# Kernel tuning notes

Measured on AMD Instinct MI355X. Metric: run time of the kernel, lower is better.

## Reference

```python
import jax, jax.numpy as jnp
import numpy as np

N, T, V = 256, 70, 64
B, H, C = 6, 1024, 4  # n_blocks, n_internal_units, n_class
SPECTRAL_RADIUS = 0.99
INPUT_SCALING = 0.2


def setup_inputs() -> dict:
    key = jax.random.key(0)
    k1, k2, k3, k4 = jax.random.split(key, 4)
    X = jax.random.normal(k1, (N, T, V), dtype=jnp.float32)
    # spectral-radius-normalized reservoir weights (circular law: rho(G/sqrt(H)) ~ 1)
    W_res = jax.random.normal(k2, (B, H, H), dtype=jnp.float32) * (SPECTRAL_RADIUS / jnp.sqrt(H).astype(jnp.float32))
    # +/-1 Bernoulli input weights scaled by input_scaling
    W_in = jnp.sign(jax.random.normal(k3, (B, H, V), dtype=jnp.float32)) * INPUT_SCALING
    W_lin = jax.random.normal(k4, (T, C, B * H), dtype=jnp.float32) * 0.02
    b_lin = jnp.zeros((T, C), dtype=jnp.float32)
    return {"X": X, "W_res": W_res, "W_in": W_in, "W_lin": W_lin, "b_lin": b_lin}


def reference(X, W_res, W_in, W_lin, b_lin):
    # Echo state recurrence: s_t = tanh(W_res @ s_{t-1} + W_in @ x_t), per block
    # (leak=None, noise_level=0.0, n_drop=0 as in module defaults)
    n, t_len, v = X.shape
    b, h, _ = W_res.shape

    def step(s, x_t):  # s: [B,N,H], x_t: [N,V]
        pre = jnp.einsum('bij,bnj->bni', W_res, s) + jnp.einsum('bhv,nv->bnh', W_in, x_t)
        s_new = jnp.tanh(pre)
        return s_new, s_new

    s0 = jnp.zeros((b, n, h), dtype=X.dtype)
    _, states = jax.lax.scan(step, s0, jnp.swapaxes(X, 0, 1))  # [T,B,N,H]

    # per-timestep features: concat blocks -> [T,N,B*H]
    feats = jnp.transpose(states, (0, 2, 1, 3)).reshape(t_len, n, b * h)
    # per-timestep linear heads
    logits = jnp.einsum('tnf,tcf->tnc', feats, W_lin) + b_lin[:, None, :]  # [T,N,C]
    preds = jnp.argmax(logits, axis=-1)  # [T,N], matches forward()'s class_dict
    return logits, preds
```

## Files before the change

### kernel.cpp

```cpp
#include <hip/hip_runtime.h>
#include <stdint.h>


typedef _Float16 f16;
typedef _Float16 f16x8 __attribute__((ext_vector_type(8)));
typedef float floatx4 __attribute__((ext_vector_type(4)));

#define N_TOT 256
#define T_TOT 70
#define V_TOT 64
#define B_TOT 6
#define H_TOT 1024
#define C_TOT 4
#define F_TOT (B_TOT * H_TOT)
#define G_TOT 192
#define LO_SCALE 4096.0f
#define LO_INV   (1.0f / 4096.0f)

union H8 { f16 h[8]; uint4 v; };

#define GLOAD16(g, l)                                                        \
    __builtin_amdgcn_global_load_lds(                                        \
        (const __attribute__((address_space(1))) void*)(g),                  \
        (__attribute__((address_space(3))) void*)(l), 16, 0, 0)

__global__ __launch_bounds__(256)
void split_f32(const float* __restrict__ src, f16* __restrict__ hi,
               f16* __restrict__ lo, int n)
{
    const int i = (blockIdx.x * 256 + threadIdx.x) * 8;
    if (i + 8 > n) return;
    const float4 a = *(const float4*)&src[i];
    const float4 b = *(const float4*)&src[i + 4];
    const float x[8] = {a.x, a.y, a.z, a.w, b.x, b.y, b.z, b.w};
    H8 H, L;
#pragma unroll
    for (int j = 0; j < 8; ++j) {
        const f16 h = (f16)x[j];
        H.h[j] = h;
        L.h[j] = (f16)((x[j] - (float)h) * LO_SCALE);
    }
    *(uint4*)&hi[i] = H.v;
    *(uint4*)&lo[i] = L.v;
}

__global__ __launch_bounds__(256)
void head_reduce(const float* __restrict__ part,
                 const float* __restrict__ b_lin,
                 float* __restrict__ logits,
                 float* __restrict__ preds)
{
    const int t = blockIdx.x;
    const int n = threadIdx.x;

    float a0 = b_lin[t * C_TOT + 0];
    float a1 = b_lin[t * C_TOT + 1];
    float a2 = b_lin[t * C_TOT + 2];
    float a3 = b_lin[t * C_TOT + 3];

    const float* p = part + (((size_t)t * G_TOT) * N_TOT + n) * C_TOT;
    for (int g = 0; g < G_TOT; ++g) {
        const float4 v = *(const float4*)&p[(size_t)g * N_TOT * C_TOT];
        a0 += v.x; a1 += v.y; a2 += v.z; a3 += v.w;
    }

    float4 o = {a0, a1, a2, a3};
    *(float4*)&logits[((size_t)t * N_TOT + n) * C_TOT] = o;

    int arg = 0;
    float best = a0;
    if (a1 > best) { best = a1; arg = 1; }
    if (a2 > best) { best = a2; arg = 2; }
    if (a3 > best) { best = a3; arg = 3; }
    preds[(size_t)t * N_TOT + n] = (float)arg;
}

__global__ __launch_bounds__(256)
void esn_step_fused(const f16* __restrict__ Xhi,   const f16* __restrict__ Xlo,
                    const f16* __restrict__ Whi,   const f16* __restrict__ Wlo,
                    const f16* __restrict__ Wihi,  const f16* __restrict__ Wilo,
                    const f16* __restrict__ shi_p, const f16* __restrict__ slo_p,
                    f16* __restrict__ shi_n,       f16* __restrict__ slo_n,
                    const float* __restrict__ W_lin, float* __restrict__ part,
                    int t, int first)
{
    __shared__ f16 As_hi[2][64 * 64];
    __shared__ f16 As_lo[2][64 * 64];
    __shared__ f16 Bs_hi[2][32 * 64];
    __shared__ f16 Bs_lo[2][32 * 64];

    const int p   = blockIdx.x;
    const int l   = (p & 7) * 96 + (p >> 3);
    const int mt  = l & 3;
    const int bi  = l >> 2;
    const int b   = bi >> 5;
    const int it  = bi & 31;

    const int tid  = threadIdx.x;
    const int w    = tid >> 6;
    const int lane = tid & 63;
    const int l16  = lane & 15;
    const int oct  = lane >> 4;
    const int r8   = lane >> 3;
    const int sw   = ((lane & 7) ^ r8) << 3;

    const int dA0 = (w * 16) * 64;
    const int dA1 = (w * 16 + 8) * 64;
    const int dB  = (w * 8) * 64;

    const int arow0 = mt * 64 + w * 16 + r8;
    const int arow1 = arow0 + 8;
    const int brow  = it * 32 + w * 8 + r8;

    const f16* Ah0 = shi_p + (size_t)(b * N_TOT + arow0) * H_TOT + sw;
    const f16* Ah1 = shi_p + (size_t)(b * N_TOT + arow1) * H_TOT + sw;
    const f16* Al0 = slo_p + (size_t)(b * N_TOT + arow0) * H_TOT + sw;
    const f16* Al1 = slo_p + (size_t)(b * N_TOT + arow1) * H_TOT + sw;
    const f16* Bh0 = Whi   + (size_t)(b * H_TOT + brow) * H_TOT + sw;
    const f16* Bl0 = Wlo   + (size_t)(b * H_TOT + brow) * H_TOT + sw;
    const f16* Xh0 = Xhi + ((size_t)arow0 * T_TOT + t) * V_TOT + sw;
    const f16* Xh1 = Xhi + ((size_t)arow1 * T_TOT + t) * V_TOT + sw;
    const f16* Xl0 = Xlo + ((size_t)arow0 * T_TOT + t) * V_TOT + sw;
    const f16* Xl1 = Xlo + ((size_t)arow1 * T_TOT + t) * V_TOT + sw;
    const f16* Wih = Wihi + (size_t)(b * H_TOT + brow) * V_TOT + sw;
    const f16* Wil = Wilo + (size_t)(b * H_TOT + brow) * V_TOT + sw;

    auto STAGE = [&](int k) {
        const int bb = k & 1;
        if (k < 16) {
            const size_t off = (size_t)k * 64;
            GLOAD16(Ah0 + off, &As_hi[bb][dA0]);
            GLOAD16(Ah1 + off, &As_hi[bb][dA1]);
            GLOAD16(Al0 + off, &As_lo[bb][dA0]);
            GLOAD16(Al1 + off, &As_lo[bb][dA1]);
            GLOAD16(Bh0 + off, &Bs_hi[bb][dB]);
            GLOAD16(Bl0 + off, &Bs_lo[bb][dB]);
        } else {
            GLOAD16(Xh0, &As_hi[bb][dA0]);
            GLOAD16(Xh1, &As_hi[bb][dA1]);
            GLOAD16(Xl0, &As_lo[bb][dA0]);
            GLOAD16(Xl1, &As_lo[bb][dA1]);
            GLOAD16(Wih, &Bs_hi[bb][dB]);
            GLOAD16(Wil, &Bs_lo[bb][dB]);
        }
    };

    floatx4 acc[2], accl[2];
#pragma unroll
    for (int j = 0; j < 2; ++j) { acc[j] = (floatx4)(0.0f); accl[j] = (floatx4)(0.0f); }

    const int xsw = (l16 & 7) << 3;
    const int aoff[2] = {
        (w * 16 + l16) * 64 + ((0 + oct * 8) ^ xsw),
        (w * 16 + l16) * 64 + ((32 + oct * 8) ^ xsw)
    };
    int boff[2][2];
#pragma unroll
    for (int nf = 0; nf < 2; ++nf) {
        boff[nf][0] = (nf * 16 + l16) * 64 + ((0 + oct * 8) ^ xsw);
        boff[nf][1] = (nf * 16 + l16) * 64 + ((32 + oct * 8) ^ xsw);
    }

    const int kc0 = first ? 16 : 0;
    STAGE(kc0);
    __syncthreads();

    for (int kc = kc0; kc <= 16; ++kc) {
        const int bb = kc & 1;
        if (kc < 16) STAGE(kc + 1);

#pragma unroll
        for (int half = 0; half < 2; ++half) {
            const f16x8 ah = *(const f16x8*)&As_hi[bb][aoff[half]];
            const f16x8 al = *(const f16x8*)&As_lo[bb][aoff[half]];
#pragma unroll
            for (int nf = 0; nf < 2; ++nf) {
                const f16x8 bh = *(const f16x8*)&Bs_hi[bb][boff[nf][half]];
                const f16x8 bl = *(const f16x8*)&Bs_lo[bb][boff[nf][half]];
                acc[nf]  = __builtin_amdgcn_mfma_f32_16x16x32_f16(ah, bh, acc[nf], 0, 0, 0);
                accl[nf] = __builtin_amdgcn_mfma_f32_16x16x32_f16(ah, bl, accl[nf], 0, 0, 0);
                accl[nf] = __builtin_amdgcn_mfma_f32_16x16x32_f16(al, bh, accl[nf], 0, 0, 0);
            }
        }
        if (kc < 16) __syncthreads();
    }

    const int nbase = mt * 64;
    const int ibase = it * 32;

    const float* wl = W_lin + (size_t)t * C_TOT * F_TOT + b * H_TOT + ibase;
    float wv[4][2];
#pragma unroll
    for (int c = 0; c < 4; ++c)
#pragma unroll
        for (int nf = 0; nf < 2; ++nf)
            wv[c][nf] = wl[(size_t)c * F_TOT + nf * 16 + l16];

    float sval[2][4];
#pragma unroll
    for (int nf = 0; nf < 2; ++nf)
#pragma unroll
        for (int r = 0; r < 4; ++r) {
            const int m  = w * 16 + oct * 4 + r;
            const int ii = nf * 16 + l16;
            const float s = tanhf(acc[nf][r] + accl[nf][r] * LO_INV);
            sval[nf][r] = s;
            const f16 h = (f16)s;
            const size_t oidx = (size_t)(b * N_TOT + nbase + m) * H_TOT + ibase + ii;
            shi_n[oidx] = h;
            slo_n[oidx] = (f16)((s - (float)h) * LO_SCALE);
        }

    const int g = b * 32 + it;
#pragma unroll
    for (int r = 0; r < 4; ++r) {
        float v[4];
#pragma unroll
        for (int c = 0; c < 4; ++c) {
            float x = sval[0][r] * wv[c][0] + sval[1][r] * wv[c][1];
            x += __shfl_xor(x, 1);
            x += __shfl_xor(x, 2);
            x += __shfl_xor(x, 4);
            x += __shfl_xor(x, 8);
            v[c] = x;
        }
        if (l16 == 0) {
            const int n = nbase + w * 16 + oct * 4 + r;
            float4 o = {v[0], v[1], v[2], v[3]};
            *(float4*)&part[(((size_t)t * G_TOT + g) * N_TOT + n) * C_TOT] = o;
        }
    }
}

extern "C" void kernel_launch(void* const* d_in, const int* in_sizes, int n_in,
                              void* d_out, int out_size, void* d_ws, size_t ws_size,
                              hipStream_t stream) {
    const float* X     = (const float*)d_in[0];
    const float* W_res = (const float*)d_in[1];
    const float* W_in  = (const float*)d_in[2];
    const float* W_lin = (const float*)d_in[3];
    const float* b_lin = (const float*)d_in[4];

    float* out    = (float*)d_out;
    float* logits = out;
    float* preds  = out + (size_t)T_TOT * N_TOT * C_TOT;

    const size_t nWres = (size_t)B_TOT * H_TOT * H_TOT;
    const size_t nWin  = (size_t)B_TOT * H_TOT * V_TOT;
    const size_t nX    = (size_t)N_TOT * T_TOT * V_TOT;
    const size_t nS    = (size_t)B_TOT * N_TOT * H_TOT;

    f16* p    = (f16*)d_ws;
    f16* Whi  = p;  p += nWres;
    f16* Wlo  = p;  p += nWres;
    f16* Wihi = p;  p += nWin;
    f16* Wilo = p;  p += nWin;
    f16* Xhi  = p;  p += nX;
    f16* Xlo  = p;  p += nX;
    f16* sAh  = p;  p += nS;
    f16* sAl  = p;  p += nS;
    f16* sBh  = p;  p += nS;
    f16* sBl  = p;  p += nS;
    float* part = (float*)p;

    split_f32<<<(int)(nWres / 2048), 256, 0, stream>>>(W_res, Whi, Wlo, (int)nWres);
    split_f32<<<(int)(nWin  / 2048), 256, 0, stream>>>(W_in, Wihi, Wilo, (int)nWin);
    split_f32<<<(int)(nX    / 2048), 256, 0, stream>>>(X, Xhi, Xlo, (int)nX);

    for (int t = 0; t < T_TOT; ++t) {
        const f16 *ph, *pl;
        f16 *nh, *nl;
        if (t & 1) { ph = sBh; pl = sBl; nh = sAh; nl = sAl; }
        else       { ph = sAh; pl = sAl; nh = sBh; nl = sBl; }
        esn_step_fused<<<B_TOT * 4 * 32, 256, 0, stream>>>(
            Xhi, Xlo, Whi, Wlo, Wihi, Wilo, ph, pl, nh, nl,
            W_lin, part, t, t == 0 ? 1 : 0);
    }
    head_reduce<<<T_TOT, 256, 0, stream>>>(part, b_lin, logits, preds);
}
```

Baseline: 1.511 ms.

## Enlarge per-block tile to 64x64 with 2-wave blocks and 2x4 MFMA fragments

```diff
diff --git a/kernel.cpp b/kernel.cpp
--- a/kernel.cpp
+++ b/kernel.cpp
@@ -75,7 +75,8 @@
     preds[(size_t)t * N_TOT + n] = (float)arg;
 }
 
-__global__ __launch_bounds__(256)
+__global__ __launch_bounds__(128)
+__attribute__((amdgpu_waves_per_eu(1, 2)))
 void esn_step_fused(const f16* __restrict__ Xhi,   const f16* __restrict__ Xlo,
                     const f16* __restrict__ Whi,   const f16* __restrict__ Wlo,
                     const f16* __restrict__ Wihi,  const f16* __restrict__ Wilo,
@@ -86,15 +87,15 @@
 {
     __shared__ f16 As_hi[2][64 * 64];
     __shared__ f16 As_lo[2][64 * 64];
-    __shared__ f16 Bs_hi[2][32 * 64];
-    __shared__ f16 Bs_lo[2][32 * 64];
+    __shared__ f16 Bs_hi[2][64 * 64];
+    __shared__ f16 Bs_lo[2][64 * 64];
 
     const int p   = blockIdx.x;
-    const int l   = (p & 7) * 96 + (p >> 3);
+    const int l   = (p & 7) * 48 + (p >> 3);
     const int mt  = l & 3;
     const int bi  = l >> 2;
-    const int b   = bi >> 5;
-    const int it  = bi & 31;
+    const int b   = bi >> 4;
+    const int it  = bi & 15;
 
     const int tid  = threadIdx.x;
     const int w    = tid >> 6;
@@ -104,62 +105,53 @@
     const int r8   = lane >> 3;
     const int sw   = ((lane & 7) ^ r8) << 3;
 
-    const int dA0 = (w * 16) * 64;
-    const int dA1 = (w * 16 + 8) * 64;
-    const int dB  = (w * 8) * 64;
-
-    const int arow0 = mt * 64 + w * 16 + r8;
-    const int arow1 = arow0 + 8;
-    const int brow  = it * 32 + w * 8 + r8;
-
-    const f16* Ah0 = shi_p + (size_t)(b * N_TOT + arow0) * H_TOT + sw;
-    const f16* Ah1 = shi_p + (size_t)(b * N_TOT + arow1) * H_TOT + sw;
-    const f16* Al0 = slo_p + (size_t)(b * N_TOT + arow0) * H_TOT + sw;
-    const f16* Al1 = slo_p + (size_t)(b * N_TOT + arow1) * H_TOT + sw;
-    const f16* Bh0 = Whi   + (size_t)(b * H_TOT + brow) * H_TOT + sw;
-    const f16* Bl0 = Wlo   + (size_t)(b * H_TOT + brow) * H_TOT + sw;
-    const f16* Xh0 = Xhi + ((size_t)arow0 * T_TOT + t) * V_TOT + sw;
-    const f16* Xh1 = Xhi + ((size_t)arow1 * T_TOT + t) * V_TOT + sw;
-    const f16* Xl0 = Xlo + ((size_t)arow0 * T_TOT + t) * V_TOT + sw;
-    const f16* Xl1 = Xlo + ((size_t)arow1 * T_TOT + t) * V_TOT + sw;
-    const f16* Wih = Wihi + (size_t)(b * H_TOT + brow) * V_TOT + sw;
-    const f16* Wil = Wilo + (size_t)(b * H_TOT + brow) * V_TOT + sw;
+    const f16* Ah  = shi_p + (size_t)(b * N_TOT + mt * 64 + w * 32 + r8) * H_TOT + sw;
+    const f16* Al  = slo_p + (size_t)(b * N_TOT + mt * 64 + w * 32 + r8) * H_TOT + sw;
+    const f16* Bh  = Whi   + (size_t)(b * H_TOT + it * 64 + w * 32 + r8) * H_TOT + sw;
+    const f16* Bl  = Wlo   + (size_t)(b * H_TOT + it * 64 + w * 32 + r8) * H_TOT + sw;
+    const f16* Xh  = Xhi + ((size_t)(mt * 64 + w * 32 + r8) * T_TOT + t) * V_TOT + sw;
+    const f16* Xl  = Xlo + ((size_t)(mt * 64 + w * 32 + r8) * T_TOT + t) * V_TOT + sw;
+    const f16* Wih = Wihi + (size_t)(b * H_TOT + it * 64 + w * 32 + r8) * V_TOT + sw;
+    const f16* Wil = Wilo + (size_t)(b * H_TOT + it * 64 + w * 32 + r8) * V_TOT + sw;
 
     auto STAGE = [&](int k) {
         const int bb = k & 1;
         if (k < 16) {
             const size_t off = (size_t)k * 64;
-            GLOAD16(Ah0 + off, &As_hi[bb][dA0]);
-            GLOAD16(Ah1 + off, &As_hi[bb][dA1]);
-            GLOAD16(Al0 + off, &As_lo[bb][dA0]);
-            GLOAD16(Al1 + off, &As_lo[bb][dA1]);
-            GLOAD16(Bh0 + off, &Bs_hi[bb][dB]);
-            GLOAD16(Bl0 + off, &Bs_lo[bb][dB]);
+#pragma unroll
+            for (int s = 0; s < 4; ++s) {
+                const int d = (w * 32 + s * 8) * 64;
+                GLOAD16(Ah + (size_t)s * 8 * H_TOT + off, &As_hi[bb][d]);
+                GLOAD16(Al + (size_t)s * 8 * H_TOT + off, &As_lo[bb][d]);
+                GLOAD16(Bh + (size_t)s * 8 * H_TOT + off, &Bs_hi[bb][d]);
+                GLOAD16(Bl + (size_t)s * 8 * H_TOT + off, &Bs_lo[bb][d]);
+            }
         } else {
-            GLOAD16(Xh0, &As_hi[bb][dA0]);
-            GLOAD16(Xh1, &As_hi[bb][dA1]);
-            GLOAD16(Xl0, &As_lo[bb][dA0]);
-            GLOAD16(Xl1, &As_lo[bb][dA1]);
-            GLOAD16(Wih, &Bs_hi[bb][dB]);
-            GLOAD16(Wil, &Bs_lo[bb][dB]);
+#pragma unroll
+            for (int s = 0; s < 4; ++s) {
+                const int d = (w * 32 + s * 8) * 64;
+                GLOAD16(Xh  + (size_t)s * 8 * T_TOT * V_TOT, &As_hi[bb][d]);
+                GLOAD16(Xl  + (size_t)s * 8 * T_TOT * V_TOT, &As_lo[bb][d]);
+                GLOAD16(Wih + (size_t)s * 8 * V_TOT,         &Bs_hi[bb][d]);
+                GLOAD16(Wil + (size_t)s * 8 * V_TOT,         &Bs_lo[bb][d]);
+            }
         }
     };
 
-    floatx4 acc[2], accl[2];
-#pragma unroll
-    for (int j = 0; j < 2; ++j) { acc[j] = (floatx4)(0.0f); accl[j] = (floatx4)(0.0f); }
+    floatx4 acc[2][4], accl[2][4];
+#pragma unroll
+    for (int m = 0; m < 2; ++m)
+#pragma unroll
+        for (int nf = 0; nf < 4; ++nf) {
+            acc[m][nf] = (floatx4)(0.0f);
+            accl[m][nf] = (floatx4)(0.0f);
+        }
 
     const int xsw = (l16 & 7) << 3;
-    const int aoff[2] = {
-        (w * 16 + l16) * 64 + ((0 + oct * 8) ^ xsw),
-        (w * 16 + l16) * 64 + ((32 + oct * 8) ^ xsw)
-    };
-    int boff[2][2];
-#pragma unroll
-    for (int nf = 0; nf < 2; ++nf) {
-        boff[nf][0] = (nf * 16 + l16) * 64 + ((0 + oct * 8) ^ xsw);
-        boff[nf][1] = (nf * 16 + l16) * 64 + ((32 + oct * 8) ^ xsw);
-    }
+    const int arow_lds[2] = { (w * 32 + l16) * 64, (w * 32 + 16 + l16) * 64 };
+    const int brow_lds[4] = { l16 * 64, (16 + l16) * 64,
+                              (32 + l16) * 64, (48 + l16) * 64 };
+    const int colk[2] = { (0 + oct * 8) ^ xsw, (32 + oct * 8) ^ xsw };
 
     const int kc0 = first ? 16 : 0;
     STAGE(kc0);
@@ -171,64 +163,79 @@
 
 #pragma unroll
         for (int half = 0; half < 2; ++half) {
-            const f16x8 ah = *(const f16x8*)&As_hi[bb][aoff[half]];
-            const f16x8 al = *(const f16x8*)&As_lo[bb][aoff[half]];
-#pragma unroll
-            for (int nf = 0; nf < 2; ++nf) {
-                const f16x8 bh = *(const f16x8*)&Bs_hi[bb][boff[nf][half]];
-                const f16x8 bl = *(const f16x8*)&Bs_lo[bb][boff[nf][half]];
-                acc[nf]  = __builtin_amdgcn_mfma_f32_16x16x32_f16(ah, bh, acc[nf], 0, 0, 0);
-                accl[nf] = __builtin_amdgcn_mfma_f32_16x16x32_f16(ah, bl, accl[nf], 0, 0, 0);
-                accl[nf] = __builtin_amdgcn_mfma_f32_16x16x32_f16(al, bh, accl[nf], 0, 0, 0);
+            f16x8 ah[2], al[2];
+#pragma unroll
+            for (int m = 0; m < 2; ++m) {
+                ah[m] = *(const f16x8*)&As_hi[bb][arow_lds[m] + colk[half]];
+                al[m] = *(const f16x8*)&As_lo[bb][arow_lds[m] + colk[half]];
+            }
+#pragma unroll
+            for (int nf = 0; nf < 4; ++nf) {
+                const f16x8 bh = *(const f16x8*)&Bs_hi[bb][brow_lds[nf] + colk[half]];
+                const f16x8 bl = *(const f16x8*)&Bs_lo[bb][brow_lds[nf] + colk[half]];
+#pragma unroll
+                for (int m = 0; m < 2; ++m) {
+                    acc[m][nf]  = __builtin_amdgcn_mfma_f32_16x16x32_f16(ah[m], bh, acc[m][nf], 0, 0, 0);
+                    accl[m][nf] = __builtin_amdgcn_mfma_f32_16x16x32_f16(ah[m], bl, accl[m][nf], 0, 0, 0);
+                    accl[m][nf] = __builtin_amdgcn_mfma_f32_16x16x32_f16(al[m], bh, accl[m][nf], 0, 0, 0);
+                }
             }
         }
         if (kc < 16) __syncthreads();
     }
 
     const int nbase = mt * 64;
-    const int ibase = it * 32;
+    const int ibase = it * 64;
 
     const float* wl = W_lin + (size_t)t * C_TOT * F_TOT + b * H_TOT + ibase;
-    float wv[4][2];
+    float wv[4][4];
 #pragma unroll
     for (int c = 0; c < 4; ++c)
 #pragma unroll
-        for (int nf = 0; nf < 2; ++nf)
+        for (int nf = 0; nf < 4; ++nf)
             wv[c][nf] = wl[(size_t)c * F_TOT + nf * 16 + l16];
 
-    float sval[2][4];
-#pragma unroll
-    for (int nf = 0; nf < 2; ++nf)
-#pragma unroll
-        for (int r = 0; r < 4; ++r) {
-            const int m  = w * 16 + oct * 4 + r;
-            const int ii = nf * 16 + l16;
-            const float s = tanhf(acc[nf][r] + accl[nf][r] * LO_INV);
-            sval[nf][r] = s;
-            const f16 h = (f16)s;
-            const size_t oidx = (size_t)(b * N_TOT + nbase + m) * H_TOT + ibase + ii;
-            shi_n[oidx] = h;
-            slo_n[oidx] = (f16)((s - (float)h) * LO_SCALE);
-        }
-
-    const int g = b * 32 + it;
-#pragma unroll
-    for (int r = 0; r < 4; ++r) {
-        float v[4];
-#pragma unroll
-        for (int c = 0; c < 4; ++c) {
-            float x = sval[0][r] * wv[c][0] + sval[1][r] * wv[c][1];
-            x += __shfl_xor(x, 1);
-            x += __shfl_xor(x, 2);
-            x += __shfl_xor(x, 4);
-            x += __shfl_xor(x, 8);
-            v[c] = x;
-        }
-        if (l16 == 0) {
-            const int n = nbase + w * 16 + oct * 4 + r;
-            float4 o = {v[0], v[1], v[2], v[3]};
-            *(float4*)&part[(((size_t)t * G_TOT + g) * N_TOT + n) * C_TOT] = o;
-        }
+    float sval[2][4][4];
+#pragma unroll
+    for (int m = 0; m < 2; ++m)
+#pragma unroll
+        for (int nf = 0; nf < 4; ++nf)
+#pragma unroll
+            for (int r = 0; r < 4; ++r) {
+                const int mrow = w * 32 + m * 16 + oct * 4 + r;
+                const int ii   = nf * 16 + l16;
+                const float s = tanhf(acc[m][nf][r] + accl[m][nf][r] * LO_INV);
+                sval[m][nf][r] = s;
+                const f16 h = (f16)s;
+                const size_t oidx = (size_t)(b * N_TOT + nbase + mrow) * H_TOT + ibase + ii;
+                shi_n[oidx] = h;
+                slo_n[oidx] = (f16)((s - (float)h) * LO_SCALE);
+            }
+
+#pragma unroll
+    for (int cg = 0; cg < 2; ++cg) {
+        const int g = b * 32 + it * 2 + cg;
+#pragma unroll
+        for (int m = 0; m < 2; ++m)
+#pragma unroll
+            for (int r = 0; r < 4; ++r) {
+                float v[4];
+#pragma unroll
+                for (int c = 0; c < 4; ++c) {
+                    float x = sval[m][2 * cg][r] * wv[c][2 * cg]
+                            + sval[m][2 * cg + 1][r] * wv[c][2 * cg + 1];
+                    x += __shfl_xor(x, 1);
+                    x += __shfl_xor(x, 2);
+                    x += __shfl_xor(x, 4);
+                    x += __shfl_xor(x, 8);
+                    v[c] = x;
+                }
+                if (l16 == 0) {
+                    const int n = nbase + w * 32 + m * 16 + oct * 4 + r;
+                    float4 o = {v[0], v[1], v[2], v[3]};
+                    *(float4*)&part[(((size_t)t * G_TOT + g) * N_TOT + n) * C_TOT] = o;
+                }
+            }
     }
 }
 
@@ -272,7 +279,7 @@
         f16 *nh, *nl;
         if (t & 1) { ph = sBh; pl = sBl; nh = sAh; nl = sAl; }
         else       { ph = sAh; pl = sAl; nh = sBh; nl = sBl; }
-        esn_step_fused<<<B_TOT * 4 * 32, 256, 0, stream>>>(
+        esn_step_fused<<<B_TOT * 16 * 4, 128, 0, stream>>>(
             Xhi, Xlo, Whi, Wlo, Wihi, Wilo, ph, pl, nh, nl,
             W_lin, part, t, t == 0 ? 1 : 0);
     }
```

New measurement: 2.305 ms. 52.6% more time.

## Interleave W hi/lo chunks and deepen the LDS pipeline to four stages

Applied to the files above, without the earlier changes.

```diff
diff --git a/kernel.cpp b/kernel.cpp
--- a/kernel.cpp
+++ b/kernel.cpp
@@ -24,6 +24,14 @@
         (const __attribute__((address_space(1))) void*)(g),                  \
         (__attribute__((address_space(3))) void*)(l), 16, 0, 0)
 
+#define LDSBAR(N)                                                            \
+    do {                                                                     \
+        __builtin_amdgcn_sched_barrier(0);                                   \
+        asm volatile("s_waitcnt vmcnt(" #N ") lgkmcnt(0)" ::: "memory");     \
+        __builtin_amdgcn_s_barrier();                                        \
+        __builtin_amdgcn_sched_barrier(0);                                   \
+    } while (0)
+
 __global__ __launch_bounds__(256)
 void split_f32(const float* __restrict__ src, f16* __restrict__ hi,
                f16* __restrict__ lo, int n)
@@ -45,6 +53,29 @@
 }
 
 __global__ __launch_bounds__(256)
+void csplit32(const float* __restrict__ src, f16* __restrict__ dst,
+              int n, int K)
+{
+    const int i = (blockIdx.x * 256 + threadIdx.x) * 8;
+    if (i + 8 > n) return;
+    const float4 a = *(const float4*)&src[i];
+    const float4 b = *(const float4*)&src[i + 4];
+    const float x[8] = {a.x, a.y, a.z, a.w, b.x, b.y, b.z, b.w};
+    H8 H, L;
+#pragma unroll
+    for (int j = 0; j < 8; ++j) {
+        const f16 h = (f16)x[j];
+        H.h[j] = h;
+        L.h[j] = (f16)((x[j] - (float)h) * LO_SCALE);
+    }
+    const int row = i / K;
+    const int k   = i - row * K;
+    const size_t o = ((size_t)row * (K >> 5) + (k >> 5)) * 64 + (k & 31);
+    *(uint4*)&dst[o]      = H.v;
+    *(uint4*)&dst[o + 32] = L.v;
+}
+
+__global__ __launch_bounds__(256)
 void head_reduce(const float* __restrict__ part,
                  const float* __restrict__ b_lin,
                  float* __restrict__ logits,
@@ -77,17 +108,15 @@
 
 __global__ __launch_bounds__(256)
 void esn_step_fused(const f16* __restrict__ Xhi,   const f16* __restrict__ Xlo,
-                    const f16* __restrict__ Whi,   const f16* __restrict__ Wlo,
-                    const f16* __restrict__ Wihi,  const f16* __restrict__ Wilo,
+                    const f16* __restrict__ Wc,    const f16* __restrict__ Wic,
                     const f16* __restrict__ shi_p, const f16* __restrict__ slo_p,
                     f16* __restrict__ shi_n,       f16* __restrict__ slo_n,
                     const float* __restrict__ W_lin, float* __restrict__ part,
                     int t, int first)
 {
-    __shared__ f16 As_hi[2][64 * 64];
-    __shared__ f16 As_lo[2][64 * 64];
-    __shared__ f16 Bs_hi[2][32 * 64];
-    __shared__ f16 Bs_lo[2][32 * 64];
+    __shared__ f16 As_hi[4][64 * 32];
+    __shared__ f16 As_lo[4][64 * 32];
+    __shared__ f16 Bs[4][32 * 64];
 
     const int p   = blockIdx.x;
     const int l   = (p & 7) * 96 + (p >> 3);
@@ -101,47 +130,32 @@
     const int lane = tid & 63;
     const int l16  = lane & 15;
     const int oct  = lane >> 4;
-    const int r8   = lane >> 3;
-    const int sw   = ((lane & 7) ^ r8) << 3;
-
-    const int dA0 = (w * 16) * 64;
-    const int dA1 = (w * 16 + 8) * 64;
-    const int dB  = (w * 8) * 64;
-
-    const int arow0 = mt * 64 + w * 16 + r8;
-    const int arow1 = arow0 + 8;
-    const int brow  = it * 32 + w * 8 + r8;
-
-    const f16* Ah0 = shi_p + (size_t)(b * N_TOT + arow0) * H_TOT + sw;
-    const f16* Ah1 = shi_p + (size_t)(b * N_TOT + arow1) * H_TOT + sw;
-    const f16* Al0 = slo_p + (size_t)(b * N_TOT + arow0) * H_TOT + sw;
-    const f16* Al1 = slo_p + (size_t)(b * N_TOT + arow1) * H_TOT + sw;
-    const f16* Bh0 = Whi   + (size_t)(b * H_TOT + brow) * H_TOT + sw;
-    const f16* Bl0 = Wlo   + (size_t)(b * H_TOT + brow) * H_TOT + sw;
-    const f16* Xh0 = Xhi + ((size_t)arow0 * T_TOT + t) * V_TOT + sw;
-    const f16* Xh1 = Xhi + ((size_t)arow1 * T_TOT + t) * V_TOT + sw;
-    const f16* Xl0 = Xlo + ((size_t)arow0 * T_TOT + t) * V_TOT + sw;
-    const f16* Xl1 = Xlo + ((size_t)arow1 * T_TOT + t) * V_TOT + sw;
-    const f16* Wih = Wihi + (size_t)(b * H_TOT + brow) * V_TOT + sw;
-    const f16* Wil = Wilo + (size_t)(b * H_TOT + brow) * V_TOT + sw;
+
+    const int arow = tid >> 2;
+    const int acg  = ((tid & 3) ^ ((tid >> 3) & 3)) << 3;
+    const int brow = tid >> 3;
+    const int bcg  = ((tid & 7) ^ ((tid >> 3) & 7)) << 3;
+
+    const f16* Asrc_h = shi_p + (size_t)(b * N_TOT + mt * 64 + arow) * H_TOT + acg;
+    const f16* Asrc_l = slo_p + (size_t)(b * N_TOT + mt * 64 + arow) * H_TOT + acg;
+    const f16* Bsrc   = Wc  + ((size_t)(b * H_TOT + it * 32 + brow) * 32) * 64 + bcg;
+    const f16* Xsrc_h = Xhi + ((size_t)(mt * 64 + arow) * T_TOT + t) * V_TOT + acg;
+    const f16* Xsrc_l = Xlo + ((size_t)(mt * 64 + arow) * T_TOT + t) * V_TOT + acg;
+    const f16* Wisrc  = Wic + ((size_t)(b * H_TOT + it * 32 + brow) * 2) * 64 + bcg;
+
+    const int dst = w * 512;
 
     auto STAGE = [&](int k) {
-        const int bb = k & 1;
-        if (k < 16) {
-            const size_t off = (size_t)k * 64;
-            GLOAD16(Ah0 + off, &As_hi[bb][dA0]);
-            GLOAD16(Ah1 + off, &As_hi[bb][dA1]);
-            GLOAD16(Al0 + off, &As_lo[bb][dA0]);
-            GLOAD16(Al1 + off, &As_lo[bb][dA1]);
-            GLOAD16(Bh0 + off, &Bs_hi[bb][dB]);
-            GLOAD16(Bl0 + off, &Bs_lo[bb][dB]);
+        const int bb = k & 3;
+        if (k < 32) {
+            GLOAD16(Asrc_h + k * 32, &As_hi[bb][dst]);
+            GLOAD16(Asrc_l + k * 32, &As_lo[bb][dst]);
+            GLOAD16(Bsrc + k * 64,   &Bs[bb][dst]);
         } else {
-            GLOAD16(Xh0, &As_hi[bb][dA0]);
-            GLOAD16(Xh1, &As_hi[bb][dA1]);
-            GLOAD16(Xl0, &As_lo[bb][dA0]);
-            GLOAD16(Xl1, &As_lo[bb][dA1]);
-            GLOAD16(Wih, &Bs_hi[bb][dB]);
-            GLOAD16(Wil, &Bs_lo[bb][dB]);
+            const int kc2 = k - 32;
+            GLOAD16(Xsrc_h + kc2 * 32, &As_hi[bb][dst]);
+            GLOAD16(Xsrc_l + kc2 * 32, &As_lo[bb][dst]);
+            GLOAD16(Wisrc + kc2 * 64,  &Bs[bb][dst]);
         }
     };
 
@@ -149,40 +163,44 @@
 #pragma unroll
     for (int j = 0; j < 2; ++j) { acc[j] = (floatx4)(0.0f); accl[j] = (floatx4)(0.0f); }
 
-    const int xsw = (l16 & 7) << 3;
-    const int aoff[2] = {
-        (w * 16 + l16) * 64 + ((0 + oct * 8) ^ xsw),
-        (w * 16 + l16) * 64 + ((32 + oct * 8) ^ xsw)
+    const int aoff = (w * 16 + l16) * 32 + ((oct ^ ((l16 >> 1) & 3)) << 3);
+    const int bx   = (l16 & 7) << 3;
+    int bhoff[2], bloff[2];
+#pragma unroll
+    for (int nf = 0; nf < 2; ++nf) {
+        bhoff[nf] = (nf * 16 + l16) * 64 + ((oct * 8) ^ bx);
+        bloff[nf] = (nf * 16 + l16) * 64 + ((32 + oct * 8) ^ bx);
+    }
+
+    auto COMPUTE = [&](int bb) {
+        const f16x8 ah = *(const f16x8*)&As_hi[bb][aoff];
+        const f16x8 al = *(const f16x8*)&As_lo[bb][aoff];
+#pragma unroll
+        for (int nf = 0; nf < 2; ++nf) {
+            const f16x8 bh = *(const f16x8*)&Bs[bb][bhoff[nf]];
+            const f16x8 bl = *(const f16x8*)&Bs[bb][bloff[nf]];
+            acc[nf]  = __builtin_amdgcn_mfma_f32_16x16x32_f16(ah, bh, acc[nf], 0, 0, 0);
+            accl[nf] = __builtin_amdgcn_mfma_f32_16x16x32_f16(ah, bl, accl[nf], 0, 0, 0);
+            accl[nf] = __builtin_amdgcn_mfma_f32_16x16x32_f16(al, bh, accl[nf], 0, 0, 0);
+        }
     };
-    int boff[2][2];
-#pragma unroll
-    for (int nf = 0; nf < 2; ++nf) {
-        boff[nf][0] = (nf * 16 + l16) * 64 + ((0 + oct * 8) ^ xsw);
-        boff[nf][1] = (nf * 16 + l16) * 64 + ((32 + oct * 8) ^ xsw);
-    }
-
-    const int kc0 = first ? 16 : 0;
-    STAGE(kc0);
-    __syncthreads();
-
-    for (int kc = kc0; kc <= 16; ++kc) {
-        const int bb = kc & 1;
-        if (kc < 16) STAGE(kc + 1);
-
-#pragma unroll
-        for (int half = 0; half < 2; ++half) {
-            const f16x8 ah = *(const f16x8*)&As_hi[bb][aoff[half]];
-            const f16x8 al = *(const f16x8*)&As_lo[bb][aoff[half]];
-#pragma unroll
-            for (int nf = 0; nf < 2; ++nf) {
-                const f16x8 bh = *(const f16x8*)&Bs_hi[bb][boff[nf][half]];
-                const f16x8 bl = *(const f16x8*)&Bs_lo[bb][boff[nf][half]];
-                acc[nf]  = __builtin_amdgcn_mfma_f32_16x16x32_f16(ah, bh, acc[nf], 0, 0, 0);
-                accl[nf] = __builtin_amdgcn_mfma_f32_16x16x32_f16(ah, bl, accl[nf], 0, 0, 0);
-                accl[nf] = __builtin_amdgcn_mfma_f32_16x16x32_f16(al, bh, accl[nf], 0, 0, 0);
-            }
-        }
-        if (kc < 16) __syncthreads();
+
+    if (!first) {
+        STAGE(0); STAGE(1); STAGE(2);
+        LDSBAR(6);
+        for (int kc = 0; kc < 31; ++kc) {
+            STAGE(kc + 3);
+            COMPUTE(kc & 3);
+            LDSBAR(6);
+        }
+        COMPUTE(31 & 3); LDSBAR(3);
+        COMPUTE(32 & 3); LDSBAR(0);
+        COMPUTE(33 & 3);
+    } else {
+        STAGE(32); STAGE(33);
+        LDSBAR(3);
+        COMPUTE(32 & 3); LDSBAR(0);
+        COMPUTE(33 & 3);
     }
 
     const int nbase = mt * 64;
@@ -251,10 +269,8 @@
     const size_t nS    = (size_t)B_TOT * N_TOT * H_TOT;
 
     f16* p    = (f16*)d_ws;
-    f16* Whi  = p;  p += nWres;
-    f16* Wlo  = p;  p += nWres;
-    f16* Wihi = p;  p += nWin;
-    f16* Wilo = p;  p += nWin;
+    f16* Wc   = p;  p += nWres * 2;
+    f16* Wic  = p;  p += nWin * 2;
     f16* Xhi  = p;  p += nX;
     f16* Xlo  = p;  p += nX;
     f16* sAh  = p;  p += nS;
@@ -263,9 +279,9 @@
     f16* sBl  = p;  p += nS;
     float* part = (float*)p;
 
-    split_f32<<<(int)(nWres / 2048), 256, 0, stream>>>(W_res, Whi, Wlo, (int)nWres);
-    split_f32<<<(int)(nWin  / 2048), 256, 0, stream>>>(W_in, Wihi, Wilo, (int)nWin);
-    split_f32<<<(int)(nX    / 2048), 256, 0, stream>>>(X, Xhi, Xlo, (int)nX);
+    csplit32<<<(int)(nWres / 2048), 256, 0, stream>>>(W_res, Wc, (int)nWres, H_TOT);
+    csplit32<<<(int)(nWin  / 2048), 256, 0, stream>>>(W_in, Wic, (int)nWin, V_TOT);
+    split_f32<<<(int)(nX   / 2048), 256, 0, stream>>>(X, Xhi, Xlo, (int)nX);
 
     for (int t = 0; t < T_TOT; ++t) {
         const f16 *ph, *pl;
@@ -273,7 +289,7 @@
         if (t & 1) { ph = sBh; pl = sBl; nh = sAh; nl = sAl; }
         else       { ph = sAh; pl = sAl; nh = sBh; nl = sBl; }
         esn_step_fused<<<B_TOT * 4 * 32, 256, 0, stream>>>(
-            Xhi, Xlo, Whi, Wlo, Wihi, Wilo, ph, pl, nh, nl,
+            Xhi, Xlo, Wc, Wic, ph, pl, nh, nl,
             W_lin, part, t, t == 0 ? 1 : 0);
     }
     head_reduce<<<T_TOT, 256, 0, stream>>>(part, b_lin, logits, preds);
```

After: 1.883 ms. +24.6%, slower.

## Switch step kernel to 32x32x16 MFMA with two waves per 64x32 tile

Applied to the files above, without the earlier changes.

```diff
diff --git a/kernel.cpp b/kernel.cpp
--- a/kernel.cpp
+++ b/kernel.cpp
@@ -4,7 +4,7 @@
 
 typedef _Float16 f16;
 typedef _Float16 f16x8 __attribute__((ext_vector_type(8)));
-typedef float floatx4 __attribute__((ext_vector_type(4)));
+typedef float floatx16 __attribute__((ext_vector_type(16)));
 
 #define N_TOT 256
 #define T_TOT 70
@@ -75,7 +75,8 @@
     preds[(size_t)t * N_TOT + n] = (float)arg;
 }
 
-__global__ __launch_bounds__(256)
+__global__ __launch_bounds__(128)
+__attribute__((amdgpu_waves_per_eu(1, 2)))
 void esn_step_fused(const f16* __restrict__ Xhi,   const f16* __restrict__ Xlo,
                     const f16* __restrict__ Whi,   const f16* __restrict__ Wlo,
                     const f16* __restrict__ Wihi,  const f16* __restrict__ Wilo,
@@ -99,67 +100,71 @@
     const int tid  = threadIdx.x;
     const int w    = tid >> 6;
     const int lane = tid & 63;
-    const int l16  = lane & 15;
-    const int oct  = lane >> 4;
+    const int l32  = lane & 31;
+    const int hi   = lane >> 5;
     const int r8   = lane >> 3;
     const int sw   = ((lane & 7) ^ r8) << 3;
 
-    const int dA0 = (w * 16) * 64;
-    const int dA1 = (w * 16 + 8) * 64;
-    const int dB  = (w * 8) * 64;
-
-    const int arow0 = mt * 64 + w * 16 + r8;
-    const int arow1 = arow0 + 8;
-    const int brow  = it * 32 + w * 8 + r8;
-
-    const f16* Ah0 = shi_p + (size_t)(b * N_TOT + arow0) * H_TOT + sw;
-    const f16* Ah1 = shi_p + (size_t)(b * N_TOT + arow1) * H_TOT + sw;
-    const f16* Al0 = slo_p + (size_t)(b * N_TOT + arow0) * H_TOT + sw;
-    const f16* Al1 = slo_p + (size_t)(b * N_TOT + arow1) * H_TOT + sw;
-    const f16* Bh0 = Whi   + (size_t)(b * H_TOT + brow) * H_TOT + sw;
-    const f16* Bl0 = Wlo   + (size_t)(b * H_TOT + brow) * H_TOT + sw;
-    const f16* Xh0 = Xhi + ((size_t)arow0 * T_TOT + t) * V_TOT + sw;
-    const f16* Xh1 = Xhi + ((size_t)arow1 * T_TOT + t) * V_TOT + sw;
-    const f16* Xl0 = Xlo + ((size_t)arow0 * T_TOT + t) * V_TOT + sw;
-    const f16* Xl1 = Xlo + ((size_t)arow1 * T_TOT + t) * V_TOT + sw;
-    const f16* Wih = Wihi + (size_t)(b * H_TOT + brow) * V_TOT + sw;
-    const f16* Wil = Wilo + (size_t)(b * H_TOT + brow) * V_TOT + sw;
+    const f16* Ah  = shi_p + (size_t)(b * N_TOT + mt * 64 + w * 32 + r8) * H_TOT + sw;
+    const f16* Al  = slo_p + (size_t)(b * N_TOT + mt * 64 + w * 32 + r8) * H_TOT + sw;
+    const f16* Bh  = Whi   + (size_t)(b * H_TOT + it * 32 + w * 16 + r8) * H_TOT + sw;
+    const f16* Bl  = Wlo   + (size_t)(b * H_TOT + it * 32 + w * 16 + r8) * H_TOT + sw;
+    const f16* Xh  = Xhi + ((size_t)(mt * 64 + w * 32 + r8) * T_TOT + t) * V_TOT + sw;
+    const f16* Xl  = Xlo + ((size_t)(mt * 64 + w * 32 + r8) * T_TOT + t) * V_TOT + sw;
+    const f16* Wih = Wihi + (size_t)(b * H_TOT + it * 32 + w * 16 + r8) * V_TOT + sw;
+    const f16* Wil = Wilo + (size_t)(b * H_TOT + it * 32 + w * 16 + r8) * V_TOT + sw;
 
     auto STAGE = [&](int k) {
         const int bb = k & 1;
         if (k < 16) {
             const size_t off = (size_t)k * 64;
-            GLOAD16(Ah0 + off, &As_hi[bb][dA0]);
-            GLOAD16(Ah1 + off, &As_hi[bb][dA1]);
-            GLOAD16(Al0 + off, &As_lo[bb][dA0]);
-            GLOAD16(Al1 + off, &As_lo[bb][dA1]);
-            GLOAD16(Bh0 + off, &Bs_hi[bb][dB]);
-            GLOAD16(Bl0 + off, &Bs_lo[bb][dB]);
+#pragma unroll
+            for (int s = 0; s < 2; ++s) {
+                GLOAD16(Bh + (size_t)(s * 8) * H_TOT + off, &Bs_hi[bb][(w * 16 + s * 8) * 64]);
+                GLOAD16(Bl + (size_t)(s * 8) * H_TOT + off, &Bs_lo[bb][(w * 16 + s * 8) * 64]);
+            }
+#pragma unroll
+            for (int s = 0; s < 4; ++s) {
+                GLOAD16(Ah + (size_t)(s * 8) * H_TOT + off, &As_hi[bb][(w * 32 + s * 8) * 64]);
+                GLOAD16(Al + (size_t)(s * 8) * H_TOT + off, &As_lo[bb][(w * 32 + s * 8) * 64]);
+            }
         } else {
-            GLOAD16(Xh0, &As_hi[bb][dA0]);
-            GLOAD16(Xh1, &As_hi[bb][dA1]);
-            GLOAD16(Xl0, &As_lo[bb][dA0]);
-            GLOAD16(Xl1, &As_lo[bb][dA1]);
-            GLOAD16(Wih, &Bs_hi[bb][dB]);
-            GLOAD16(Wil, &Bs_lo[bb][dB]);
+#pragma unroll
+            for (int s = 0; s < 2; ++s) {
+                GLOAD16(Wih + (size_t)(s * 8) * V_TOT, &Bs_hi[bb][(w * 16 + s * 8) * 64]);
+                GLOAD16(Wil + (size_t)(s * 8) * V_TOT, &Bs_lo[bb][(w * 16 + s * 8) * 64]);
+            }
+#pragma unroll
+            for (int s = 0; s < 4; ++s) {
+                GLOAD16(Xh + (size_t)(s * 8) * T_TOT * V_TOT, &As_hi[bb][(w * 32 + s * 8) * 64]);
+                GLOAD16(Xl + (size_t)(s * 8) * T_TOT * V_TOT, &As_lo[bb][(w * 32 + s * 8) * 64]);
+            }
         }
     };
 
-    floatx4 acc[2], accl[2];
-#pragma unroll
-    for (int j = 0; j < 2; ++j) { acc[j] = (floatx4)(0.0f); accl[j] = (floatx4)(0.0f); }
-
-    const int xsw = (l16 & 7) << 3;
-    const int aoff[2] = {
-        (w * 16 + l16) * 64 + ((0 + oct * 8) ^ xsw),
-        (w * 16 + l16) * 64 + ((32 + oct * 8) ^ xsw)
+    floatx16 acc = (floatx16)(0.0f);
+    floatx16 accl = (floatx16)(0.0f);
+
+    const int abase = (w * 32 + l32) * 64;
+    const int bbase = l32 * 64;
+    const int gx    = (lane & 7) << 3;
+    int koff[4];
+#pragma unroll
+    for (int q = 0; q < 4; ++q)
+        koff[q] = (((2 * q + hi) << 3) ^ gx);
+
+    auto COMPUTE = [&](int bb) {
+#pragma unroll
+        for (int q = 0; q < 4; ++q) {
+            const f16x8 ah = *(const f16x8*)&As_hi[bb][abase + koff[q]];
+            const f16x8 al = *(const f16x8*)&As_lo[bb][abase + koff[q]];
+            const f16x8 bh = *(const f16x8*)&Bs_hi[bb][bbase + koff[q]];
+            const f16x8 bl = *(const f16x8*)&Bs_lo[bb][bbase + koff[q]];
+            acc  = __builtin_amdgcn_mfma_f32_32x32x16_f16(ah, bh, acc, 0, 0, 0);
+            accl = __builtin_amdgcn_mfma_f32_32x32x16_f16(ah, bl, accl, 0, 0, 0);
+            accl = __builtin_amdgcn_mfma_f32_32x32x16_f16(al, bh, accl, 0, 0, 0);
+        }
     };
-    int boff[2][2];
-#pragma unroll
-    for (int nf = 0; nf < 2; ++nf) {
-        boff[nf][0] = (nf * 16 + l16) * 64 + ((0 + oct * 8) ^ xsw);
-        boff[nf][1] = (nf * 16 + l16) * 64 + ((32 + oct * 8) ^ xsw);
-    }
 
     const int kc0 = first ? 16 : 0;
     STAGE(kc0);
@@ -168,20 +173,7 @@
     for (int kc = kc0; kc <= 16; ++kc) {
         const int bb = kc & 1;
         if (kc < 16) STAGE(kc + 1);
-
-#pragma unroll
-        for (int half = 0; half < 2; ++half) {
-            const f16x8 ah = *(const f16x8*)&As_hi[bb][aoff[half]];
-            const f16x8 al = *(const f16x8*)&As_lo[bb][aoff[half]];
-#pragma unroll
-            for (int nf = 0; nf < 2; ++nf) {
-                const f16x8 bh = *(const f16x8*)&Bs_hi[bb][boff[nf][half]];
-                const f16x8 bl = *(const f16x8*)&Bs_lo[bb][boff[nf][half]];
-                acc[nf]  = __builtin_amdgcn_mfma_f32_16x16x32_f16(ah, bh, acc[nf], 0, 0, 0);
-                accl[nf] = __builtin_amdgcn_mfma_f32_16x16x32_f16(ah, bl, accl[nf], 0, 0, 0);
-                accl[nf] = __builtin_amdgcn_mfma_f32_16x16x32_f16(al, bh, accl[nf], 0, 0, 0);
-            }
-        }
+        COMPUTE(bb);
         if (kc < 16) __syncthreads();
     }
 
@@ -189,43 +181,41 @@
     const int ibase = it * 32;
 
     const float* wl = W_lin + (size_t)t * C_TOT * F_TOT + b * H_TOT + ibase;
-    float wv[4][2];
+    float wv[4];
 #pragma unroll
     for (int c = 0; c < 4; ++c)
-#pragma unroll
-        for (int nf = 0; nf < 2; ++nf)
-            wv[c][nf] = wl[(size_t)c * F_TOT + nf * 16 + l16];
-
-    float sval[2][4];
-#pragma unroll
-    for (int nf = 0; nf < 2; ++nf)
-#pragma unroll
-        for (int r = 0; r < 4; ++r) {
-            const int m  = w * 16 + oct * 4 + r;
-            const int ii = nf * 16 + l16;
-            const float s = tanhf(acc[nf][r] + accl[nf][r] * LO_INV);
-            sval[nf][r] = s;
-            const f16 h = (f16)s;
-            const size_t oidx = (size_t)(b * N_TOT + nbase + m) * H_TOT + ibase + ii;
-            shi_n[oidx] = h;
-            slo_n[oidx] = (f16)((s - (float)h) * LO_SCALE);
-        }
+        wv[c] = wl[(size_t)c * F_TOT + l32];
+
+    float sval[16];
+#pragma unroll
+    for (int r = 0; r < 16; ++r) {
+        const int row = (r & 3) + 8 * (r >> 2) + 4 * hi;
+        const int m   = w * 32 + row;
+        const float s = tanhf(acc[r] + accl[r] * LO_INV);
+        sval[r] = s;
+        const f16 h = (f16)s;
+        const size_t oidx = (size_t)(b * N_TOT + nbase + m) * H_TOT + ibase + l32;
+        shi_n[oidx] = h;
+        slo_n[oidx] = (f16)((s - (float)h) * LO_SCALE);
+    }
 
     const int g = b * 32 + it;
 #pragma unroll
-    for (int r = 0; r < 4; ++r) {
+    for (int r = 0; r < 16; ++r) {
         float v[4];
 #pragma unroll
         for (int c = 0; c < 4; ++c) {
-            float x = sval[0][r] * wv[c][0] + sval[1][r] * wv[c][1];
+            float x = sval[r] * wv[c];
             x += __shfl_xor(x, 1);
             x += __shfl_xor(x, 2);
             x += __shfl_xor(x, 4);
             x += __shfl_xor(x, 8);
+            x += __shfl_xor(x, 16);
             v[c] = x;
         }
-        if (l16 == 0) {
-            const int n = nbase + w * 16 + oct * 4 + r;
+        if (l32 == 0) {
+            const int row = (r & 3) + 8 * (r >> 2) + 4 * hi;
+            const int n = nbase + w * 32 + row;
             float4 o = {v[0], v[1], v[2], v[3]};
             *(float4*)&part[(((size_t)t * G_TOT + g) * N_TOT + n) * C_TOT] = o;
         }
@@ -272,7 +262,7 @@
         f16 *nh, *nl;
         if (t & 1) { ph = sBh; pl = sBl; nh = sAh; nl = sAl; }
         else       { ph = sAh; pl = sAl; nh = sBh; nl = sBl; }
-        esn_step_fused<<<B_TOT * 4 * 32, 256, 0, stream>>>(
+        esn_step_fused<<<B_TOT * 4 * 32, 128, 0, stream>>>(
             Xhi, Xlo, Whi, Wlo, Wihi, Wilo, ph, pl, nh, nl,
             W_lin, part, t, t == 0 ? 1 : 0);
     }
```

Result: slower. 1.924 ms (+27.3%).
